# Performance work log

Hardware: AMD Instinct MI355X
Metric: run time of the kernel (lower is better)

Reference implementation:

```python
import jax, jax.numpy as jnp
import numpy as np

B, H, F = 4096, 32, 1024     # batch, hp_num, feat_dim
N_CAT, CAT_DIM = 8, 16       # categorical dims 0..7, each |domain| = 16
N_CONT = H - N_CAT
LN_EPS = 1e-5


def setup_inputs() -> dict:
    key = jax.random.key(0)
    ks = jax.random.split(key, 8)
    s = 1.0 / np.sqrt(F)  # ~xavier scale
    return {
        "z": jax.random.normal(ks[0], (B, F), jnp.float32),
        "edge": jax.random.randint(ks[1], (2, 10), 0, B),
        # stacked per-hp projection Linears (weights stored as [in, out])
        "W_proj": jax.random.normal(ks[2], (H, F, F), jnp.float32) * s,
        "b_proj": jnp.zeros((H, F), jnp.float32),
        # LayerNorm over [hp_num, feat_dim]
        "ln_w": jnp.ones((H, F), jnp.float32),
        "ln_b": jnp.zeros((H, F), jnp.float32),
        # reverse_embedding for categorical dims (softmax heads)
        "W_cat": jax.random.normal(ks[3], (N_CAT, F, CAT_DIM), jnp.float32) * s,
        "b_cat": jnp.zeros((N_CAT, CAT_DIM), jnp.float32),
        # reverse_embedding for continuous dims (scalar heads)
        "W_cont": jax.random.normal(ks[4], (N_CONT, F, 1), jnp.float32) * s,
        "b_cont": jnp.zeros((N_CONT, 1), jnp.float32),
    }


def reference(z, edge, W_proj, b_proj, ln_w, ln_b, W_cat, b_cat, W_cont, b_cont):
    # per-hp projection: batched GEMM replacing batch*hp_num tiny Linears
    latent = jnp.einsum('bf,hfd->bhd', z, W_proj) + b_proj  # [B, H, F]
    # LayerNorm normalized over the last two dims [hp_num, feat_dim]
    mu = latent.mean(axis=(1, 2), keepdims=True)
    var = latent.var(axis=(1, 2), keepdims=True)
    latent = (latent - mu) * jax.lax.rsqrt(var + LN_EPS) * ln_w + ln_b
    latent = jax.nn.relu(latent)
    # reverse embeddings: categorical heads (dims 0..N_CAT-1) get softmax
    cat_logits = jnp.einsum('bhf,hfc->bhc', latent[:, :N_CAT], W_cat) + b_cat
    pred_cat = jax.nn.softmax(cat_logits, axis=-1)          # [B, N_CAT, CAT_DIM]
    pred_cont = jnp.einsum('bhf,hfc->bhc', latent[:, N_CAT:], W_cont) + b_cont  # [B, N_CONT, 1]
    return pred_cat, pred_cont, latent
```

## Files before the change

### kernel.cpp

```cpp
#include <hip/hip_runtime.h>

typedef unsigned short u16;
typedef unsigned int u32;
typedef __bf16 bf16x8 __attribute__((ext_vector_type(8)));
typedef float f32x4 __attribute__((ext_vector_type(4)));

#define B_SZ   4096
#define H_NUM  32
#define F_DIM  1024
#define NTOT   (H_NUM * F_DIM)
#define N_CAT  8
#define CAT_D  16
#define N_CONT 24
#define LN_EPS 1e-5f
#define NSTRIP 128

__device__ __forceinline__ u16 f2bf(float f) {
    unsigned int u = __builtin_bit_cast(unsigned int, f);
    unsigned int r = (u + 0x7FFFu + ((u >> 16) & 1u)) >> 16;
    return (u16)r;
}

__device__ __forceinline__ float bf2f(u16 v) {
    unsigned int u = ((unsigned int)v) << 16;
    return __builtin_bit_cast(float, u);
}

__device__ __forceinline__ float bflo(u32 v) { return bf2f((u16)(v & 0xffffu)); }
__device__ __forceinline__ float bfhi(u32 v) { return bf2f((u16)(v >> 16)); }

__device__ __forceinline__ void gl2lds16(const void* g, void* l) {
    __builtin_amdgcn_global_load_lds(
        (const __attribute__((address_space(1))) void*)g,
        (__attribute__((address_space(3))) void*)l,
        16, 0, 0);
}

__device__ __forceinline__ float wave_sum(float v) {
#pragma unroll
    for (int o = 32; o; o >>= 1) v += __shfl_xor(v, o);
    return v;
}

__global__ __launch_bounds__(256) void zconv(const float* __restrict__ z,
                                             u16* __restrict__ zb) {
    int i = blockIdx.x * 256 + threadIdx.x;
    float4 v = ((const float4*)z)[i];
    ushort4 o;
    o.x = f2bf(v.x); o.y = f2bf(v.y); o.z = f2bf(v.z); o.w = f2bf(v.w);
    ((ushort4*)zb)[i] = o;
}

__global__ __launch_bounds__(256) void packln(const float* __restrict__ lnw,
                                              const float* __restrict__ lnb,
                                              const float* __restrict__ wcont,
                                              uint4* __restrict__ lnwb,
                                              ushort4* __restrict__ wc16) {
    int idx = blockIdx.x * 256 + threadIdx.x;
    if (idx < NTOT / 4) {
        float4 w = ((const float4*)lnw)[idx];
        float4 b = ((const float4*)lnb)[idx];
        uint4 o;
        o.x = (u32)f2bf(w.x) | ((u32)f2bf(w.y) << 16);
        o.y = (u32)f2bf(w.z) | ((u32)f2bf(w.w) << 16);
        o.z = (u32)f2bf(b.x) | ((u32)f2bf(b.y) << 16);
        o.w = (u32)f2bf(b.z) | ((u32)f2bf(b.w) << 16);
        lnwb[idx] = o;
    } else if (idx < NTOT / 4 + N_CONT * F_DIM / 4) {
        int j = idx - NTOT / 4;
        float4 v = ((const float4*)wcont)[j];
        ushort4 o;
        o.x = f2bf(v.x); o.y = f2bf(v.y); o.z = f2bf(v.z); o.w = f2bf(v.w);
        wc16[j] = o;
    }
}

__global__ __launch_bounds__(256) void transpose_w(const float* __restrict__ W,
                                                   u16* __restrict__ Wt) {
    __shared__ u16 tile[64][72];
    const int h = blockIdx.z;
    const int f0 = blockIdx.x * 64;
    const int d0 = blockIdx.y * 64;
    const float* Wh = W + (size_t)h * F_DIM * F_DIM;
    u16* Wth = Wt + (size_t)h * F_DIM * F_DIM;
    const int t = threadIdx.x;

#pragma unroll
    for (int i = 0; i < 4; ++i) {
        int idx = i * 256 + t;
        int fr = idx >> 4;
        int c4 = idx & 15;
        float4 v = *(const float4*)(Wh + (size_t)(f0 + fr) * F_DIM + d0 + c4 * 4);
        tile[fr][c4 * 4 + 0] = f2bf(v.x);
        tile[fr][c4 * 4 + 1] = f2bf(v.y);
        tile[fr][c4 * 4 + 2] = f2bf(v.z);
        tile[fr][c4 * 4 + 3] = f2bf(v.w);
    }
    __syncthreads();
#pragma unroll
    for (int i = 0; i < 2; ++i) {
        int idx = i * 256 + t;
        int dr = idx >> 3;
        int c8 = idx & 7;
        __attribute__((aligned(16))) u16 tmp[8];
#pragma unroll
        for (int j = 0; j < 8; ++j) tmp[j] = tile[c8 * 8 + j][dr];
        *(uint4*)(Wth + (size_t)(d0 + dr) * F_DIM + f0 + c8 * 8) = *(const uint4*)tmp;
    }
}

template <int BF>
__global__ __launch_bounds__(512, 2) void gemm256(const u16* __restrict__ A,
                                                  const u16* __restrict__ Bt,
                                                  const float* __restrict__ bproj,
                                                  u16* __restrict__ lat16,
                                                  float* __restrict__ latf,
                                                  float* __restrict__ psum,
                                                  float* __restrict__ psumsq) {
    extern __shared__ u16 dynlds[];
    const int t = threadIdx.x;
    const int wid = t >> 6;
    const int lane = t & 63;
    const int l16 = lane & 15;
    const int lk = lane >> 4;
    const int wm = wid >> 2;
    const int wn = wid & 3;

    const int wg = blockIdx.x;
    const int xcd = wg & 7;
    const int local = wg >> 3;
    const int m0 = (local & 15) * 256;
    const int n0 = ((xcd << 4) + (local >> 4)) * 256;

    f32x4 acc[8][4];
    const f32x4 zero = {0.f, 0.f, 0.f, 0.f};
#pragma unroll
    for (int m = 0; m < 8; ++m)
#pragma unroll
        for (int n = 0; n < 4; ++n) acc[m][n] = zero;

    auto stage = [&](int p, int ktn, int bn) {
        const char* srcbase = (p < 2) ? (const char*)A : (const char*)Bt;
        const int rowbase = (p < 2) ? (m0 + p * 128) : (n0 + (p - 2) * 128);
        u16* ldsbase = dynlds + bn * 32768 + (p >> 1) * 16384 + (p & 1) * 8192;
#pragma unroll
        for (int i = 0; i < 2; ++i) {
            int oo = i * 8192 + t * 16;
            int oos = oo ^ (((oo >> 7) & 7) << 4);
            int row = oo >> 7;
            int colb = oos & 127;
            gl2lds16(srcbase + (size_t)(rowbase + row) * 2048 + ktn * 128 + colb,
                     ldsbase + i * 4096 + (wid << 9));
        }
    };

#pragma unroll
    for (int p = 0; p < 4; ++p) stage(p, 0, 0);
    __syncthreads();

    const int swz = (l16 & 7) << 4;
    for (int kt = 0; kt < 16; ++kt) {
        const int buf = kt & 1;
        const char* aB = (const char*)(dynlds + buf * 32768 + wm * 8192);
        const char* bB = (const char*)(dynlds + buf * 32768 + 16384 + (wn >> 1) * 8192);

        if (kt < 15) {
#pragma unroll
            for (int p = 0; p < 4; ++p) stage(p, kt + 1, buf ^ 1);
        }

        bf16x8 bfr[4][2];
#pragma unroll
        for (int p = 0; p < 4; ++p) {
            if (p == 0) {
#pragma unroll
                for (int nr = 0; nr < 4; ++nr)
#pragma unroll
                    for (int kk = 0; kk < 2; ++kk)
                        bfr[nr][kk] = *(const bf16x8*)(bB +
                            ((wn & 1) * 64 + nr * 16 + l16) * 128 +
                            ((kk * 64 + lk * 16) ^ swz));
            }
            bf16x8 afr[2][2];
#pragma unroll
            for (int mr = 0; mr < 2; ++mr)
#pragma unroll
                for (int kk = 0; kk < 2; ++kk)
                    afr[mr][kk] = *(const bf16x8*)(aB +
                        (p * 32 + mr * 16 + l16) * 128 +
                        ((kk * 64 + lk * 16) ^ swz));
            __builtin_amdgcn_s_setprio(1);
#pragma unroll
            for (int kk = 0; kk < 2; ++kk)
#pragma unroll
                for (int mr = 0; mr < 2; ++mr)
#pragma unroll
                    for (int nr = 0; nr < 4; ++nr)
                        acc[p * 2 + mr][nr] = __builtin_amdgcn_mfma_f32_16x16x32_bf16(
                            afr[mr][kk], bfr[nr][kk], acc[p * 2 + mr][nr], 0, 0, 0);
            __builtin_amdgcn_s_setprio(0);
        }
        __syncthreads();
    }

    float bias[4];
#pragma unroll
    for (int nr = 0; nr < 4; ++nr) bias[nr] = bproj[n0 + wn * 64 + nr * 16 + l16];

    float sm[8][4], s2[8][4];
#pragma unroll
    for (int mr = 0; mr < 8; ++mr)
#pragma unroll
        for (int j = 0; j < 4; ++j) { sm[mr][j] = 0.f; s2[mr][j] = 0.f; }

#pragma unroll
    for (int mr = 0; mr < 8; ++mr) {
#pragma unroll
        for (int j = 0; j < 4; ++j) {
            const int rowg = m0 + wm * 128 + mr * 16 + lk * 4 + j;
            size_t off = (size_t)rowg * NTOT + n0 + wn * 64 + l16;
#pragma unroll
            for (int nr = 0; nr < 4; ++nr) {
                float v = acc[mr][nr][j] + bias[nr];
                if (BF) lat16[off + nr * 16] = f2bf(v);
                else    latf[off + nr * 16] = v;
                sm[mr][j] += v;
                s2[mr][j] += v * v;
            }
        }
    }
#pragma unroll
    for (int o = 1; o < 16; o <<= 1) {
#pragma unroll
        for (int mr = 0; mr < 8; ++mr)
#pragma unroll
            for (int j = 0; j < 4; ++j) {
                sm[mr][j] += __shfl_xor(sm[mr][j], o);
                s2[mr][j] += __shfl_xor(s2[mr][j], o);
            }
    }
    float* sredf = (float*)dynlds;
    float* s2f   = sredf + 1024;
    __syncthreads();
    if (l16 == 0) {
#pragma unroll
        for (int mr = 0; mr < 8; ++mr)
#pragma unroll
            for (int j = 0; j < 4; ++j) {
                int r = wm * 128 + mr * 16 + lk * 4 + j;
                sredf[wn * 256 + r] = sm[mr][j];
                s2f[wn * 256 + r] = s2[mr][j];
            }
    }
    __syncthreads();
    if (t < 256) {
        const int strip = n0 >> 8;
        float S = sredf[t] + sredf[256 + t] + sredf[512 + t] + sredf[768 + t];
        float S2 = s2f[t] + s2f[256 + t] + s2f[512 + t] + s2f[768 + t];
        psum[(size_t)strip * B_SZ + m0 + t] = S;
        psumsq[(size_t)strip * B_SZ + m0 + t] = S2;
    }
}

__global__ __launch_bounds__(256) void ln_finalize(const float* __restrict__ psum,
                                                   const float* __restrict__ psumsq,
                                                   float* __restrict__ murs) {
    const int t = threadIdx.x;
    const int b0 = blockIdx.x * 64;
    const int tb = t & 63;
    const int tg = t >> 6;
    float s = 0.f, s2 = 0.f;
    for (int sidx = tg; sidx < NSTRIP; sidx += 4) {
        s += psum[(size_t)sidx * B_SZ + b0 + tb];
        s2 += psumsq[(size_t)sidx * B_SZ + b0 + tb];
    }
    __shared__ float r1[4][64], r2[4][64];
    r1[tg][tb] = s;
    r2[tg][tb] = s2;
    __syncthreads();
    if (t < 64) {
        float S = r1[0][t] + r1[1][t] + r1[2][t] + r1[3][t];
        float S2 = r2[0][t] + r2[1][t] + r2[2][t] + r2[3][t];
        float m = S / (float)NTOT;
        float var = S2 / (float)NTOT - m * m;
        murs[b0 + t] = m;
        murs[B_SZ + b0 + t] = rsqrtf(var + LN_EPS);
    }
}

#define CONT_GROUP(G0)                                                        \
    {                                                                         \
        float cp8[8];                                                         \
        _Pragma("unroll")                                                     \
        for (int j = 0; j < 8; ++j) {                                         \
            const int k = N_CAT + (G0) + j;                                   \
            const int i = (k << 8) + t;                                       \
            float4 x;                                                         \
            if (BF) {                                                         \
                ushort4 xv = lin16[i];                                        \
                x.x = bf2f(xv.x); x.y = bf2f(xv.y);                           \
                x.z = bf2f(xv.z); x.w = bf2f(xv.w);                           \
            } else {                                                          \
                x = linf[i];                                                  \
            }                                                                 \
            uint4 wb = lnwb[i];                                               \
            ushort4 wv = wc16[(((G0) + j) << 8) + t];                         \
            float4 yo;                                                        \
            yo.x = fmaxf(0.f, (x.x - mu) * rs * bflo(wb.x) + bflo(wb.z));     \
            yo.y = fmaxf(0.f, (x.y - mu) * rs * bfhi(wb.x) + bfhi(wb.z));     \
            yo.z = fmaxf(0.f, (x.z - mu) * rs * bflo(wb.y) + bflo(wb.w));     \
            yo.w = fmaxf(0.f, (x.w - mu) * rs * bfhi(wb.y) + bfhi(wb.w));     \
            lout4[i] = yo;                                                    \
            cp8[j] = yo.x * bf2f(wv.x) + yo.y * bf2f(wv.y) +                  \
                     yo.z * bf2f(wv.z) + yo.w * bf2f(wv.w);                   \
        }                                                                     \
        _Pragma("unroll")                                                     \
        for (int j = 0; j < 8; ++j) {                                         \
            float v = wave_sum(cp8[j]);                                       \
            if (lane == 0) nred[(G0) + j][w4] = v;                            \
        }                                                                     \
    }

template <int BF>
__global__ __launch_bounds__(256) void headsK(const void* __restrict__ latin_,
                                              float* __restrict__ latout,
                                              const float* __restrict__ murs,
                                              const uint4* __restrict__ lnwb,
                                              const ushort4* __restrict__ wc16,
                                              const float* __restrict__ Wcat,
                                              const float* __restrict__ bcat,
                                              const float* __restrict__ bcont,
                                              float* __restrict__ pcat,
                                              float* __restrict__ pcont) {
    const int b = blockIdx.x;
    const int t = threadIdx.x;
    const int lane = t & 63;
    const int w4 = t >> 6;
    const float mu = murs[b];
    const float rs = murs[B_SZ + b];
    const ushort4* lin16 = (const ushort4*)((const u16*)latin_ + (size_t)b * NTOT);
    const float4*  linf  = (const float4*)((const float*)latin_ + (size_t)b * NTOT);
    float4* lout4 = (float4*)(latout + (size_t)b * NTOT);

    __shared__ ushort4 sy16[N_CAT * 256];
    __shared__ float4 cred4[4][N_CAT][4];
    __shared__ float nred[N_CONT][4];

#pragma unroll 2
    for (int k = 0; k < N_CAT; ++k) {
        const int i = (k << 8) + t;
        float4 x;
        if (BF) {
            ushort4 xv = lin16[i];
            x.x = bf2f(xv.x); x.y = bf2f(xv.y); x.z = bf2f(xv.z); x.w = bf2f(xv.w);
        } else {
            x = linf[i];
        }
        uint4 wb = lnwb[i];
        float4 yo;
        yo.x = fmaxf(0.f, (x.x - mu) * rs * bflo(wb.x) + bflo(wb.z));
        yo.y = fmaxf(0.f, (x.y - mu) * rs * bfhi(wb.x) + bfhi(wb.z));
        yo.z = fmaxf(0.f, (x.z - mu) * rs * bflo(wb.y) + bflo(wb.w));
        yo.w = fmaxf(0.f, (x.w - mu) * rs * bfhi(wb.y) + bfhi(wb.w));
        lout4[i] = yo;
        ushort4 ys;
        ys.x = f2bf(yo.x); ys.y = f2bf(yo.y); ys.z = f2bf(yo.z); ys.w = f2bf(yo.w);
        sy16[i] = ys;
    }

    CONT_GROUP(0)
    CONT_GROUP(8)
    CONT_GROUP(16)
    __syncthreads();

    const int cq = t & 3;
    const int fg = t >> 2;
    for (int k = 0; k < N_CAT; ++k) {
        const float4* Wc4 = (const float4*)(Wcat + (size_t)k * F_DIM * CAT_D);
        float4 a4 = {0.f, 0.f, 0.f, 0.f};
#pragma unroll
        for (int jq = 0; jq < 4; ++jq) {
            ushort4 yv = sy16[(k << 8) + fg * 4 + jq];
            float ys[4] = {bf2f(yv.x), bf2f(yv.y), bf2f(yv.z), bf2f(yv.w)};
#pragma unroll
            for (int r = 0; r < 4; ++r) {
                int f = fg * 16 + jq * 4 + r;
                float4 wv = Wc4[f * 4 + cq];
                a4.x += ys[r] * wv.x;
                a4.y += ys[r] * wv.y;
                a4.z += ys[r] * wv.z;
                a4.w += ys[r] * wv.w;
            }
        }
#pragma unroll
        for (int o = 4; o < 64; o <<= 1) {
            a4.x += __shfl_xor(a4.x, o);
            a4.y += __shfl_xor(a4.y, o);
            a4.z += __shfl_xor(a4.z, o);
            a4.w += __shfl_xor(a4.w, o);
        }
        if (lane < 4) cred4[w4][k][lane] = a4;
    }
    __syncthreads();

    if (t < 128) {
        const int h = t >> 4, c = t & 15;
        float lg = bcat[h * CAT_D + c];
#pragma unroll
        for (int w = 0; w < 4; ++w)
            lg += ((const float*)cred4[w][h])[c];
        float mx = lg;
#pragma unroll
        for (int o = 8; o; o >>= 1) mx = fmaxf(mx, __shfl_xor(mx, o, 16));
        float e = __expf(lg - mx);
        float sm2 = e;
#pragma unroll
        for (int o = 8; o; o >>= 1) sm2 += __shfl_xor(sm2, o, 16);
        pcat[(size_t)b * (N_CAT * CAT_D) + t] = e / sm2;
    } else if (t >= 128 && t < 128 + N_CONT) {
        const int ci = t - 128;
        pcont[(size_t)b * N_CONT + ci] =
            nred[ci][0] + nred[ci][1] + nred[ci][2] + nred[ci][3] + bcont[ci];
    }
}

extern "C" void kernel_launch(void* const* d_in, const int* in_sizes, int n_in,
                              void* d_out, int out_size, void* d_ws, size_t ws_size,
                              hipStream_t stream) {
    const float* z     = (const float*)d_in[0];
    const float* Wp    = (const float*)d_in[2];
    const float* bp    = (const float*)d_in[3];
    const float* lnw   = (const float*)d_in[4];
    const float* lnb   = (const float*)d_in[5];
    const float* Wcat  = (const float*)d_in[6];
    const float* bcat  = (const float*)d_in[7];
    const float* Wcont = (const float*)d_in[8];
    const float* bcont = (const float*)d_in[9];

    float* out    = (float*)d_out;
    float* pcat   = out;
    float* pcont  = out + (size_t)B_SZ * N_CAT * CAT_D;
    float* latent = pcont + (size_t)B_SZ * N_CONT;

    u16* zb     = (u16*)d_ws;
    u16* Wt     = zb + (size_t)B_SZ * F_DIM;
    float* murs = (float*)(Wt + (size_t)NTOT * F_DIM);
    float* psum   = murs + 2 * B_SZ;
    float* psumsq = psum + (size_t)B_SZ * NSTRIP;
    uint4* lnwb = (uint4*)(psumsq + (size_t)B_SZ * NSTRIP);
    ushort4* wc16 = (ushort4*)(lnwb + NTOT / 4);
    u16* lat16  = (u16*)(wc16 + N_CONT * F_DIM / 4);

    const size_t need = (size_t)((char*)(lat16 + (size_t)B_SZ * NTOT) - (char*)d_ws);
    const bool usebf = ws_size >= need;

    const int LDSB = 131072;
    zconv<<<dim3(B_SZ * F_DIM / 1024), 256, 0, stream>>>(z, zb);
    packln<<<dim3((NTOT / 4 + N_CONT * F_DIM / 4 + 255) / 256), 256, 0, stream>>>(
        lnw, lnb, Wcont, lnwb, wc16);
    transpose_w<<<dim3(16, 16, 32), 256, 0, stream>>>(Wp, Wt);
    if (usebf) {
        (void)hipFuncSetAttribute((const void*)gemm256<1>,
                                  hipFuncAttributeMaxDynamicSharedMemorySize, LDSB);
        gemm256<1><<<dim3(2048), 512, LDSB, stream>>>(zb, Wt, bp, lat16, nullptr,
                                                      psum, psumsq);
        ln_finalize<<<dim3(B_SZ / 64), 256, 0, stream>>>(psum, psumsq, murs);
        headsK<1><<<dim3(B_SZ), 256, 0, stream>>>(lat16, latent, murs, lnwb, wc16,
                                                  Wcat, bcat, bcont, pcat, pcont);
    } else {
        (void)hipFuncSetAttribute((const void*)gemm256<0>,
                                  hipFuncAttributeMaxDynamicSharedMemorySize, LDSB);
        gemm256<0><<<dim3(2048), 512, LDSB, stream>>>(zb, Wt, bp, nullptr, latent,
                                                      psum, psumsq);
        ln_finalize<<<dim3(B_SZ / 64), 256, 0, stream>>>(psum, psumsq, murs);
        headsK<0><<<dim3(B_SZ), 256, 0, stream>>>(latent, latent, murs, lnwb, wc16,
                                                  Wcat, bcat, bcont, pcat, pcont);
    }
}
```

Before: 702.5 us.

## Deepen GEMM LDS pipeline to four buffers with K=32 steps and vmcnt waits

Restructures the main bf16 GEMM K-loop from a double-buffered K=64 step to a four-stage ring of K=32 tiles. Three tiles are prefetched ahead and explicit s_waitcnt vmcnt counts plus a single barrier per step replace the full __syncthreads, so global-to-LDS loads overlap more with MFMA work. The swizzle is adapted to 64-byte rows. In exchange there are twice as many loop iterations and barriers, and correctness depends on the hand-tuned vmcnt counts.

```diff
diff --git a/kernel.cpp b/kernel.cpp
--- a/kernel.cpp
+++ b/kernel.cpp
@@ -14,6 +14,7 @@
 #define N_CONT 24
 #define LN_EPS 1e-5f
 #define NSTRIP 128
+#define NT_KT  32
 
 __device__ __forceinline__ u16 f2bf(float f) {
     unsigned int u = __builtin_bit_cast(unsigned int, f);
@@ -118,6 +119,7 @@
                                                   float* __restrict__ psum,
                                                   float* __restrict__ psumsq) {
     extern __shared__ u16 dynlds[];
+    char* ldsb = (char*)dynlds;
     const int t = threadIdx.x;
     const int wid = t >> 6;
     const int lane = t & 63;
@@ -139,68 +141,54 @@
 #pragma unroll
         for (int n = 0; n < 4; ++n) acc[m][n] = zero;
 
-    auto stage = [&](int p, int ktn, int bn) {
-        const char* srcbase = (p < 2) ? (const char*)A : (const char*)Bt;
-        const int rowbase = (p < 2) ? (m0 + p * 128) : (n0 + (p - 2) * 128);
-        u16* ldsbase = dynlds + bn * 32768 + (p >> 1) * 16384 + (p & 1) * 8192;
-#pragma unroll
-        for (int i = 0; i < 2; ++i) {
-            int oo = i * 8192 + t * 16;
-            int oos = oo ^ (((oo >> 7) & 7) << 4);
-            int row = oo >> 7;
-            int colb = oos & 127;
-            gl2lds16(srcbase + (size_t)(rowbase + row) * 2048 + ktn * 128 + colb,
-                     ldsbase + i * 4096 + (wid << 9));
+    auto stage = [&](int ktn) {
+        const int bn = ktn & 3;
+#pragma unroll
+        for (int i = 0; i < 4; ++i) {
+            const int isB = i >> 1;
+            int oo = (i & 1) * 8192 + t * 16;
+            int row = oo >> 6;
+            int colb = (oo & 63) ^ ((row & 3) << 4);
+            const char* src = (isB ? (const char*)Bt : (const char*)A)
+                            + (size_t)((isB ? n0 : m0) + row) * 2048
+                            + (size_t)ktn * 64 + colb;
+            char* dst = ldsb + bn * 32768 + isB * 16384 + (i & 1) * 8192 + wid * 1024;
+            gl2lds16(src, dst);
         }
     };
 
-#pragma unroll
-    for (int p = 0; p < 4; ++p) stage(p, 0, 0);
-    __syncthreads();
-
-    const int swz = (l16 & 7) << 4;
-    for (int kt = 0; kt < 16; ++kt) {
-        const int buf = kt & 1;
-        const char* aB = (const char*)(dynlds + buf * 32768 + wm * 8192);
-        const char* bB = (const char*)(dynlds + buf * 32768 + 16384 + (wn >> 1) * 8192);
-
-        if (kt < 15) {
-#pragma unroll
-            for (int p = 0; p < 4; ++p) stage(p, kt + 1, buf ^ 1);
-        }
-
-        bf16x8 bfr[4][2];
-#pragma unroll
-        for (int p = 0; p < 4; ++p) {
-            if (p == 0) {
-#pragma unroll
-                for (int nr = 0; nr < 4; ++nr)
-#pragma unroll
-                    for (int kk = 0; kk < 2; ++kk)
-                        bfr[nr][kk] = *(const bf16x8*)(bB +
-                            ((wn & 1) * 64 + nr * 16 + l16) * 128 +
-                            ((kk * 64 + lk * 16) ^ swz));
-            }
-            bf16x8 afr[2][2];
-#pragma unroll
-            for (int mr = 0; mr < 2; ++mr)
-#pragma unroll
-                for (int kk = 0; kk < 2; ++kk)
-                    afr[mr][kk] = *(const bf16x8*)(aB +
-                        (p * 32 + mr * 16 + l16) * 128 +
-                        ((kk * 64 + lk * 16) ^ swz));
-            __builtin_amdgcn_s_setprio(1);
-#pragma unroll
-            for (int kk = 0; kk < 2; ++kk)
-#pragma unroll
-                for (int mr = 0; mr < 2; ++mr)
-#pragma unroll
-                    for (int nr = 0; nr < 4; ++nr)
-                        acc[p * 2 + mr][nr] = __builtin_amdgcn_mfma_f32_16x16x32_bf16(
-                            afr[mr][kk], bfr[nr][kk], acc[p * 2 + mr][nr], 0, 0, 0);
-            __builtin_amdgcn_s_setprio(0);
-        }
-        __syncthreads();
+    const int swz = (l16 & 3) << 4;
+    auto compute = [&](int ktn) {
+        const char* base = ldsb + (ktn & 3) * 32768;
+        bf16x8 bfr[4];
+#pragma unroll
+        for (int nf = 0; nf < 4; ++nf)
+            bfr[nf] = *(const bf16x8*)(base + 16384 +
+                (wn * 64 + nf * 16 + l16) * 64 + ((lk * 16) ^ swz));
+        __builtin_amdgcn_s_setprio(1);
+#pragma unroll
+        for (int mf = 0; mf < 8; ++mf) {
+            bf16x8 af = *(const bf16x8*)(base +
+                (wm * 128 + mf * 16 + l16) * 64 + ((lk * 16) ^ swz));
+#pragma unroll
+            for (int nf = 0; nf < 4; ++nf)
+                acc[mf][nf] = __builtin_amdgcn_mfma_f32_16x16x32_bf16(
+                    af, bfr[nf], acc[mf][nf], 0, 0, 0);
+        }
+        __builtin_amdgcn_s_setprio(0);
+    };
+
+    stage(0);
+    stage(1);
+    stage(2);
+
+    for (int kt = 0; kt < NT_KT; ++kt) {
+        if (kt < NT_KT - 2)      asm volatile("s_waitcnt vmcnt(8)" ::: "memory");
+        else if (kt == NT_KT - 2) asm volatile("s_waitcnt vmcnt(4)" ::: "memory");
+        else                      asm volatile("s_waitcnt vmcnt(0)" ::: "memory");
+        __builtin_amdgcn_s_barrier();
+        if (kt + 3 < NT_KT) stage(kt + 3);
+        compute(kt);
     }
 
     float bias[4];
```

New measurement: 724.4 us. +3.1%, slower.
